# Optimization experiments

Hardware: AMD Instinct MI355X
Metric: run time of the kernel (lower is better)

## Reference

```python
import jax, jax.numpy as jnp
import numpy as np
from jax import lax


def _instance_loss(z1, z2, t):
    # z1, z2: [B,T,C]; t: [B,T] timestamps
    B, T, C = z1.shape
    if B == 1:
        return jnp.asarray(0.0, z1.dtype)
    N = B * T
    tf = t.reshape(N)
    diff = jnp.abs(tf[:, None] - tf[None, :])          # [N,N]
    seq = jnp.repeat(jnp.arange(B), T)                 # sequence id per row
    same_seq = seq[:, None] == seq[None, :]
    diff = jnp.where(same_seq, diff + diff.max() + 0.001, diff)
    # k=B smallest diffs per row (cross-sequence temporal neighbors)
    _, idx = lax.top_k(-diff, B)                       # [N,B]
    z1f = z1.reshape(N, C)
    z2f = z2.reshape(N, C)
    pos = jnp.sum(z1f * z2f, axis=-1)[:, None]         # [N,1]
    neg1 = jnp.einsum('nc,nkc->nk', z1f, z1f[idx])     # [N,B]
    neg2 = jnp.einsum('nc,nkc->nk', z1f, z2f[idx])     # [N,B]
    logits = jnp.concatenate([pos, neg1, neg2], axis=1)
    return -jax.nn.log_softmax(logits, axis=1)[:, 0].mean()


def _temporal_loss(z1, z2):
    B, T, C = z1.shape
    if T == 1:
        return jnp.asarray(0.0, z1.dtype)
    z = jnp.concatenate([z1, z2], axis=1)              # [B,2T,C]
    n = 2 * T
    sim = jnp.einsum('bic,bjc->bij', z, z)             # [B,2T,2T]
    # tril(sim,-1)[:,:,:-1] + triu(sim,1)[:,:,1:] == drop-diagonal shift
    i = jnp.arange(n)[:, None]
    j = jnp.arange(n - 1)[None, :]
    logits = jnp.where(j < i, sim[:, :, : n - 1], sim[:, :, 1:])  # [B,2T,2T-1]
    nls = -jax.nn.log_softmax(logits, axis=-1)
    tt = jnp.arange(T)
    return (nls[:, tt, T + tt - 1].mean() + nls[:, T + tt, tt].mean()) / 2


def _max_pool2(z):
    # F.max_pool1d(kernel=2, stride=2) over time axis (floor, drops odd tail)
    B, T, C = z.shape
    T2 = T // 2
    return z[:, : 2 * T2].reshape(B, T2, 2, C).max(axis=2)


def hierarchical_contrastive_loss(z1, z2, t, alpha=0.5, temporal_unit=0):
    B = z1.shape[0]
    loss = jnp.asarray(0.0, z1.dtype)
    d = 0
    while z1.shape[1] > 1:
        if alpha != 0:
            loss = loss + alpha * _instance_loss(z1, z2, t)
        if d >= temporal_unit and (1 - alpha) != 0:
            loss = loss + (1 - alpha) * _temporal_loss(z1, z2)
        d += 1
        z1 = _max_pool2(z1)
        z2 = _max_pool2(z2)
        Tt = t.shape[1]
        if Tt % 2 != 0:
            t = t[:, :-1]
        t = t.reshape(B, -1, 2).mean(axis=2)
    if z1.shape[1] == 1:
        if alpha != 0:
            loss = loss + alpha * _instance_loss(z1, z2, t)
        d += 1
    return loss / d


def setup_inputs() -> dict:
    key = jax.random.key(0)
    k1, k2, k3 = jax.random.split(key, 3)
    B, T, C = 8, 512, 320
    z1 = jax.random.normal(k1, (B, T, C), dtype=jnp.float32)
    z2 = jax.random.normal(k2, (B, T, C), dtype=jnp.float32)
    # irregular, increasing timestamps per sequence
    t = jnp.sort(jax.random.uniform(k3, (B, T), dtype=jnp.float32) * T, axis=1)
    return {"z1": z1, "z2": z2, "t": t}


def reference(z1, z2, t):
    return hierarchical_contrastive_loss(z1, z2, t, alpha=0.5, temporal_unit=0)
```

## Files before the change

kernel.cpp:

```cpp
#include <hip/hip_runtime.h>
#include <math.h>

#define BB 8
#define CC 320
#define ZB 2618880
#define TTOT 4088
#define NROWS 8184
#define NROWS_T 16352
#define NTBLK 440
#define PTOT 88032
#define XTOT 8176
#define NP1 327680
#define NP2 5120

#define FT 2618880
#define FPART 2622968
#define FROW 2799032
#define FCROSS 2823568

constexpr int kT[10]       = {512,256,128,64,32,16,8,4,2,1};
constexpr int kLogT[10]    = {9,8,7,6,5,4,3,2,1,0};
constexpr int kZBoff[10]   = {0,1310720,1966080,2293760,2457600,2539520,2580480,2600960,2611200,2616320};
constexpr int kToff[10]    = {0,0,2048,3072,3584,3840,3968,4032,4064,4080};
constexpr int kRowcum[11]  = {0,4096,6144,7168,7680,7936,8064,8128,8160,8176,8184};
constexpr int kTRowcum[10] = {0,8192,12288,14336,15360,15872,16128,16256,16320,16352};
constexpr int kNt128[9]    = {8,4,2,1,1,1,1,1,1};
constexpr int kLog128[9]   = {3,2,1,0,0,0,0,0,0};
constexpr int kPoff128[9]  = {0,65536,81920,86016,87040,87552,87808,87936,88000};
constexpr int kScount[9]   = {36,10,3,1,1,1,1,1,1};
constexpr int kSblkcum[10] = {0,288,368,392,400,408,416,424,432,440};
constexpr int kXoff[9]     = {0,4096,6144,7168,7680,7936,8064,8128,8160};

typedef short v8s __attribute__((ext_vector_type(8)));
typedef float v16f __attribute__((ext_vector_type(16)));

__device__ __forceinline__ unsigned short f2bf(float x) {
    unsigned int u = __float_as_uint(x);
    u = (u + 0x7FFFu + ((u >> 16) & 1u)) >> 16;
    return (unsigned short)u;
}
__device__ __forceinline__ float bfu(unsigned short u) {
    return __uint_as_float(((unsigned int)u) << 16);
}

__global__ void pool_lvl03(const float* __restrict__ z1,
                           const float* __restrict__ z2,
                           const float* __restrict__ t,
                           unsigned short* __restrict__ zb,
                           float* __restrict__ tpool) {
    int gid = blockIdx.x * 256 + threadIdx.x;
    if (gid < NP1) {
        int c = gid % CC;
        int rest = gid / CC;
        int ch = rest & 63;
        int b = (rest >> 6) & 7;
        int which = rest >> 9;
        const float* src =
            (which ? z2 : z1) + ((size_t)(b * 512 + ch * 8)) * CC + c;
        unsigned short* dst = zb + (size_t)which * ZB;
        float v[8];
#pragma unroll
        for (int j = 0; j < 8; j++) v[j] = src[(size_t)j * CC];
#pragma unroll
        for (int j = 0; j < 8; j++)
            dst[(size_t)(b * 512 + ch * 8 + j) * CC + c] = f2bf(v[j]);
        float m1[4];
#pragma unroll
        for (int j = 0; j < 4; j++) m1[j] = fmaxf(v[2 * j], v[2 * j + 1]);
#pragma unroll
        for (int j = 0; j < 4; j++)
            dst[kZBoff[1] + (size_t)(b * 256 + ch * 4 + j) * CC + c] =
                f2bf(m1[j]);
        float m2[2] = {fmaxf(m1[0], m1[1]), fmaxf(m1[2], m1[3])};
#pragma unroll
        for (int j = 0; j < 2; j++)
            dst[kZBoff[2] + (size_t)(b * 128 + ch * 2 + j) * CC + c] =
                f2bf(m2[j]);
        dst[kZBoff[3] + (size_t)(b * 64 + ch) * CC + c] =
            f2bf(fmaxf(m2[0], m2[1]));
    } else if (gid < NP1 + TTOT) {
        int i = gid - NP1;
        int l = 1;
#pragma unroll
        for (int q = 2; q <= 9; q++) l = (i >= kToff[q]) ? q : l;
        int rem = i - kToff[l];
        int Tl = kT[l];
        int t2 = rem & (Tl - 1);
        int b = rem >> kLogT[l];
        int win = 512 / Tl;
        const float* p = t + b * 512 + t2 * win;
        float s = 0.f;
        for (int j = 0; j < win; j++) s += p[j];
        tpool[kToff[l] + rem] = s * (1.0f / win);
    }
}

__global__ void pool_lvl49(unsigned short* __restrict__ zb) {
    int gid = blockIdx.x * 256 + threadIdx.x;
    if (gid >= NP2) return;
    int c = gid % CC;
    int r2 = gid / CC;
    int b = r2 & 7;
    int which = r2 >> 3;
    unsigned short* base = zb + (size_t)which * ZB;
    const unsigned short* src = base + kZBoff[3] + (size_t)(b * 64) * CC + c;
    float a[32];
#pragma unroll
    for (int j = 0; j < 32; j++)
        a[j] = fmaxf(bfu(src[(size_t)(2 * j) * CC]),
                     bfu(src[(size_t)(2 * j + 1) * CC]));
#pragma unroll
    for (int j = 0; j < 32; j++)
        base[kZBoff[4] + (size_t)(b * 32 + j) * CC + c] = f2bf(a[j]);
#pragma unroll
    for (int j = 0; j < 16; j++) a[j] = fmaxf(a[2 * j], a[2 * j + 1]);
#pragma unroll
    for (int j = 0; j < 16; j++)
        base[kZBoff[5] + (size_t)(b * 16 + j) * CC + c] = f2bf(a[j]);
#pragma unroll
    for (int j = 0; j < 8; j++) a[j] = fmaxf(a[2 * j], a[2 * j + 1]);
#pragma unroll
    for (int j = 0; j < 8; j++)
        base[kZBoff[6] + (size_t)(b * 8 + j) * CC + c] = f2bf(a[j]);
#pragma unroll
    for (int j = 0; j < 4; j++) a[j] = fmaxf(a[2 * j], a[2 * j + 1]);
#pragma unroll
    for (int j = 0; j < 4; j++)
        base[kZBoff[7] + (size_t)(b * 4 + j) * CC + c] = f2bf(a[j]);
#pragma unroll
    for (int j = 0; j < 2; j++) a[j] = fmaxf(a[2 * j], a[2 * j + 1]);
#pragma unroll
    for (int j = 0; j < 2; j++)
        base[kZBoff[8] + (size_t)(b * 2 + j) * CC + c] = f2bf(a[j]);
    base[kZBoff[9] + (size_t)b * CC + c] = f2bf(fmaxf(a[0], a[1]));
}

__global__ void topk_inst_all(const unsigned short* __restrict__ zb,
                              const float* __restrict__ t0,
                              const float* __restrict__ tpool,
                              float* __restrict__ rowloss) {
    int wave = threadIdx.x >> 6, lane = threadIdx.x & 63;
    int row = blockIdx.x * 4 + wave;
    if (row >= NROWS) return;
    int l = 0;
#pragma unroll
    for (int q = 1; q <= 9; q++) l = (row >= kRowcum[q]) ? q : l;
    int n = row - kRowcum[l];
    int T = kT[l];
    const float* tt = l ? tpool + kToff[l] : t0;
    int seq = n >> kLogT[l];
    float tn = tt[n];

    int idx8[8];
    if (lane < 8) {
        const float* ts = tt + lane * T;
        bool own = (lane == seq);
        int lo = 0, hi = T;
        while (lo < hi) {
            int mid = (lo + hi) >> 1;
            if (ts[mid] < tn) lo = mid + 1; else hi = mid;
        }
        int il = lo - 1, ih = lo;
        float dl = (il >= 0) ? (tn - ts[il]) : 3.0e38f;
        float dh = (ih < T) ? (ts[ih] - tn) : 3.0e38f;
#pragma unroll
        for (int r = 0; r < 8; r++) {
            bool pickLo = (dl <= dh);
            float dmin = own ? 1.0e12f : (pickLo ? dl : dh);
            int midx = own ? n : (lane * T + (pickLo ? il : ih));
            unsigned long long key =
                ((unsigned long long)__float_as_uint(dmin) << 32) |
                (unsigned int)midx;
            unsigned long long o;
            o = __shfl_xor(key, 1); key = (key < o) ? key : o;
            o = __shfl_xor(key, 2); key = (key < o) ? key : o;
            o = __shfl_xor(key, 4); key = (key < o) ? key : o;
            int widx = (int)(unsigned int)(key & 0xffffffffull);
            idx8[r] = widx;
            if (!own && widx == midx) {
                if (pickLo) { il--; dl = (il >= 0) ? (tn - ts[il]) : 3.0e38f; }
                else        { ih++; dh = (ih < T)  ? (ts[ih] - tn) : 3.0e38f; }
            }
        }
    }

    const unsigned short* z1 = zb + kZBoff[l];
    const unsigned short* z2 = zb + ZB + kZBoff[l];
    const unsigned short* z1n = z1 + (size_t)n * CC;
    const unsigned short* z2n = z2 + (size_t)n * CC;
    float a[5];
#pragma unroll
    for (int j = 0; j < 5; j++) a[j] = bfu(z1n[lane + 64 * j]);
    float part[17];
    {
        float s = 0.f;
#pragma unroll
        for (int j = 0; j < 5; j++) s += a[j] * bfu(z2n[lane + 64 * j]);
        part[0] = s;
    }
#pragma unroll
    for (int k = 0; k < 8; k++) {
        int p = __shfl(idx8[k], 0);
        const unsigned short* r1 = z1 + (size_t)p * CC;
        const unsigned short* r2 = z2 + (size_t)p * CC;
        float s1 = 0.f, s2 = 0.f;
#pragma unroll
        for (int j = 0; j < 5; j++) {
            float av = a[j];
            s1 += av * bfu(r1[lane + 64 * j]);
            s2 += av * bfu(r2[lane + 64 * j]);
        }
        part[1 + k] = s1;
        part[9 + k] = s2;
    }
#pragma unroll
    for (int q = 0; q < 17; q++) {
        float v = part[q];
        for (int off = 32; off > 0; off >>= 1) v += __shfl_xor(v, off);
        part[q] = v;
    }
    if (lane == 0) {
        float m = part[0];
#pragma unroll
        for (int q = 1; q < 17; q++) m = fmaxf(m, part[q]);
        float s = 0.f;
#pragma unroll
        for (int q = 0; q < 17; q++) s += expf(part[q] - m);
        float w = 0.05f / (float)(BB * T);
        rowloss[row] = w * (m + logf(s) - part[0]);
    }
}

__global__ void __launch_bounds__(256) temporal_mfma(
        const unsigned short* __restrict__ zb, float2* __restrict__ part,
        float* __restrict__ crossbuf) {
    int bid = blockIdx.x;
    int l = 0;
#pragma unroll
    for (int q = 1; q <= 8; q++) l = (bid >= kSblkcum[q]) ? q : l;
    int rem = bid - kSblkcum[l];
    int cnt = kScount[l];
    int Tl = kT[l], n = 2 * Tl, lnt = kLog128[l];
    int b = rem / cnt;
    int pr = rem - b * cnt;
    int rt = 0, width = kNt128[l];
    while (pr >= width) { pr -= width; rt++; width--; }
    int ct = rt + pr;
    bool diag = (rt == ct);
    const unsigned short* zb1 = zb + kZBoff[l] + (size_t)b * Tl * CC;
    const unsigned short* zb2 = zb + ZB + kZBoff[l] + (size_t)b * Tl * CC;
    int row0 = rt * 128, col0 = ct * 128;
    int tid = threadIdx.x;
    int w = tid >> 6, lane = tid & 63;
    __shared__ __align__(16) unsigned short As[4096];
    __shared__ __align__(16) unsigned short Bs[4096];
    __shared__ float2 cred[4][128];

    v16f acc[4];
#pragma unroll
    for (int cs = 0; cs < 4; cs++)
#pragma unroll
        for (int e = 0; e < 16; e++) acc[cs][e] = 0.f;

    int sofq[2]; const unsigned short* srcA[2]; const unsigned short* srcB[2];
    bool vA[2], vB[2];
#pragma unroll
    for (int q = 0; q < 2; q++) {
        int g = q * 256 + tid;
        int r = g & 127, kbb = g >> 7;
        sofq[q] = (r >> 5) * 1024 + (kbb >> 1) * 512 + (kbb & 1) * 256 +
                  (r & 31) * 8;
        int ka = kbb * 8;
        int gr = row0 + r;
        vA[q] = gr < n;
        srcA[q] = vA[q] ? ((gr < Tl) ? zb1 + (size_t)gr * CC + ka
                                     : zb2 + (size_t)(gr - Tl) * CC + ka)
                        : zb1;
        int gc = col0 + r;
        vB[q] = gc < n;
        srcB[q] = vB[q] ? ((gc < Tl) ? zb1 + (size_t)gc * CC + ka
                                     : zb2 + (size_t)(gc - Tl) * CC + ka)
                        : zb1;
    }

    for (int kc = 0; kc < CC; kc += 32) {
#pragma unroll
        for (int q = 0; q < 2; q++) {
            uint4 av = vA[q] ? *(const uint4*)(srcA[q] + kc)
                             : make_uint4(0, 0, 0, 0);
            *(uint4*)(As + sofq[q]) = av;
            if (!diag) {
                uint4 bv = vB[q] ? *(const uint4*)(srcB[q] + kc)
                                 : make_uint4(0, 0, 0, 0);
                *(uint4*)(Bs + sofq[q]) = bv;
            }
        }
        __syncthreads();
        const unsigned short* Ab = As + w * 1024;
        const unsigned short* Bb = diag ? As : Bs;
#pragma unroll
        for (int cc = 0; cc < 2; cc++) {
            v8s af = *(const v8s*)(Ab + cc * 512 + lane * 8);
#pragma unroll
            for (int cs = 0; cs < 4; cs++) {
                v8s bf = *(const v8s*)(Bb + cs * 1024 + cc * 512 + lane * 8);
                acc[cs] = __builtin_amdgcn_mfma_f32_32x32x16_bf16(
                    af, bf, acc[cs], 0, 0, 0);
            }
        }
        __syncthreads();
    }

    int colin = lane & 31;
    int rowhalf = 4 * (lane >> 5);

#pragma unroll
    for (int r = 0; r < 16; r++) {
        int lrow = (r & 3) + 8 * (r >> 2) + rowhalf;
        int grow = row0 + w * 32 + lrow;
        float vals[4];
        float lm = -3.0e38f;
#pragma unroll
        for (int cs = 0; cs < 4; cs++) {
            int gcol = col0 + cs * 32 + colin;
            float v = acc[cs][r];
            if (gcol >= n || gcol == grow) v = -3.0e38f;
            vals[cs] = v;
            lm = fmaxf(lm, v);
        }
#pragma unroll
        for (int off = 1; off < 32; off <<= 1)
            lm = fmaxf(lm, __shfl_xor(lm, off));
        float ls = 0.f;
#pragma unroll
        for (int cs = 0; cs < 4; cs++)
            ls += (vals[cs] > -1.0e38f) ? expf(vals[cs] - lm) : 0.f;
#pragma unroll
        for (int off = 1; off < 32; off <<= 1) ls += __shfl_xor(ls, off);
        if (colin == 0 && grow < n)
            part[kPoff128[l] + ((b * n + grow) << lnt) + ct] =
                make_float2(lm, ls);
    }

    if (ct - rt == (Tl >> 7)) {
#pragma unroll
        for (int r = 0; r < 16; r++) {
            int lrow = (r & 3) + 8 * (r >> 2) + rowhalf;
            int grow = row0 + w * 32 + lrow;
            if (grow < Tl) {
                int cidx = grow + Tl - col0;
                int cs_p = cidx >> 5, colin_p = cidx & 31;
                float cand = 0.f;
#pragma unroll
                for (int cs = 0; cs < 4; cs++)
                    cand += (cs == cs_p && colin == colin_p) ? acc[cs][r] : 0.f;
#pragma unroll
                for (int off = 1; off < 32; off <<= 1)
                    cand += __shfl_xor(cand, off);
                if (colin == 0)
                    crossbuf[kXoff[l] + b * Tl + grow] = cand;
            }
        }
    }

    if (!diag) {
#pragma unroll
        for (int cs = 0; cs < 4; cs++) {
            float m = acc[cs][0];
#pragma unroll
            for (int r = 1; r < 16; r++) m = fmaxf(m, acc[cs][r]);
            float mo = __shfl_xor(m, 32);
            float mm = fmaxf(m, mo);
            float s = 0.f;
#pragma unroll
            for (int r = 0; r < 16; r++) s += expf(acc[cs][r] - mm);
            s += __shfl_xor(s, 32);
            if (lane < 32) cred[w][cs * 32 + lane] = make_float2(mm, s);
        }
    }
    __syncthreads();
    if (!diag && tid < 128) {
        float2 a0 = cred[0][tid], a1 = cred[1][tid];
        float2 a2 = cred[2][tid], a3 = cred[3][tid];
        float M = fmaxf(fmaxf(a0.x, a1.x), fmaxf(a2.x, a3.x));
        float S = a0.y * expf(a0.x - M) + a1.y * expf(a1.x - M) +
                  a2.y * expf(a2.x - M) + a3.y * expf(a3.x - M);
        int gcol = col0 + tid;
        part[kPoff128[l] + ((b * n + gcol) << lnt) + rt] = make_float2(M, S);
    }
}

__global__ void merge_all(const float2* __restrict__ part,
                          const float* __restrict__ crossbuf,
                          float* __restrict__ rowloss) {
    int row = blockIdx.x * 256 + threadIdx.x;
    if (row >= NROWS_T) return;
    int l = 0;
#pragma unroll
    for (int q = 1; q <= 8; q++) l = (row >= kTRowcum[q]) ? q : l;
    int r = row - kTRowcum[l];
    int Tl = kT[l], n = 2 * Tl, nt = kNt128[l], lnt = kLog128[l];
    int b = r >> (kLogT[l] + 1);
    int rr = r & (n - 1);
    const float2* p = part + kPoff128[l] + ((size_t)(b * n + rr) << lnt);
    float M = -3.0e38f, S = 0.f;
    for (int k = 0; k < nt; k++) {
        float2 q = p[k];
        float nM = fmaxf(M, q.x);
        S = S * expf(M - nM) + q.y * expf(q.x - nM);
        M = nM;
    }
    float cross = crossbuf[kXoff[l] + b * Tl + (rr < Tl ? rr : rr - Tl)];
    float w = 0.025f / (float)(BB * Tl);
    rowloss[NROWS + row] = w * (M + logf(S) - cross);
}

__global__ void reduce_kernel(const float* __restrict__ rowloss,
                              float* __restrict__ out) {
    __shared__ float sm[16];
    int tid = threadIdx.x;
    float s = 0.f;
    for (int i = tid; i < NROWS + NROWS_T; i += 1024) s += rowloss[i];
#pragma unroll
    for (int off = 32; off > 0; off >>= 1) s += __shfl_xor(s, off);
    if ((tid & 63) == 0) sm[tid >> 6] = s;
    __syncthreads();
    if (tid < 64) {
        float v = (tid < 16) ? sm[tid] : 0.f;
#pragma unroll
        for (int off = 8; off > 0; off >>= 1) v += __shfl_xor(v, off);
        if (tid == 0) out[0] = v;
    }
}

extern "C" void kernel_launch(void* const* d_in, const int* in_sizes, int n_in,
                              void* d_out, int out_size, void* d_ws,
                              size_t ws_size, hipStream_t stream) {
    const float* z1 = (const float*)d_in[0];
    const float* z2 = (const float*)d_in[1];
    const float* t  = (const float*)d_in[2];
    float* ws = (float*)d_ws;
    unsigned short* zb = (unsigned short*)ws;
    float* tpool = ws + FT;
    float2* part = (float2*)(ws + FPART);
    float* rowloss = ws + FROW;
    float* crossbuf = ws + FCROSS;

    pool_lvl03<<<(NP1 + TTOT + 255) / 256, 256, 0, stream>>>(z1, z2, t, zb,
                                                             tpool);
    pool_lvl49<<<(NP2 + 255) / 256, 256, 0, stream>>>(zb);
    topk_inst_all<<<NROWS / 4, 256, 0, stream>>>(zb, t, tpool, rowloss);
    temporal_mfma<<<NTBLK, 256, 0, stream>>>(zb, part, crossbuf);
    merge_all<<<(NROWS_T + 255) / 256, 256, 0, stream>>>(part, crossbuf,
                                                         rowloss);
    reduce_kernel<<<1, 1024, 0, stream>>>(rowloss, (float*)d_out);
}
```

Before: 116.0 us.

## Fuse six launches into three: merged pooling, combined work kernel, last-block reduce

Folds the level 4-9 pooling into the first pooling kernel, recomputing it directly from the fp32 inputs with 16-row max windows. The temporal MFMA tiles and the instance top-k rows now run in one heterogeneous grid. Merge and final reduction use a last-block-done atomic counter. This cuts launch count and inter-kernel gaps and lets the two independent loss branches share the GPU, at the cost of more serial per-thread work in the new pooling path and an atomic counter that is reset inside the pooling kernel.

```diff
diff --git a/kernel.cpp b/kernel.cpp
--- a/kernel.cpp
+++ b/kernel.cpp
@@ -8,15 +8,16 @@
 #define NROWS 8184
 #define NROWS_T 16352
 #define NTBLK 440
-#define PTOT 88032
-#define XTOT 8176
 #define NP1 327680
 #define NP2 5120
+#define NMRB 64
 
 #define FT 2618880
 #define FPART 2622968
-#define FROW 2799032
-#define FCROSS 2823568
+#define FCROSS 2799032
+#define FROW 2807208
+#define FBLK 2815396
+#define FCNT 2815464
 
 constexpr int kT[10]       = {512,256,128,64,32,16,8,4,2,1};
 constexpr int kLogT[10]    = {9,8,7,6,5,4,3,2,1,0};
@@ -43,12 +44,14 @@
     return __uint_as_float(((unsigned int)u) << 16);
 }
 
-__global__ void pool_lvl03(const float* __restrict__ z1,
-                           const float* __restrict__ z2,
-                           const float* __restrict__ t,
-                           unsigned short* __restrict__ zb,
-                           float* __restrict__ tpool) {
+__global__ void pool_kernel(const float* __restrict__ z1,
+                            const float* __restrict__ z2,
+                            const float* __restrict__ t,
+                            unsigned short* __restrict__ zb,
+                            float* __restrict__ tpool,
+                            int* __restrict__ counter) {
     int gid = blockIdx.x * 256 + threadIdx.x;
+    if (gid == 0) *counter = 0;
     if (gid < NP1) {
         int c = gid % CC;
         int rest = gid / CC;
@@ -92,56 +95,54 @@
         float s = 0.f;
         for (int j = 0; j < win; j++) s += p[j];
         tpool[kToff[l] + rem] = s * (1.0f / win);
-    }
-}
-
-__global__ void pool_lvl49(unsigned short* __restrict__ zb) {
-    int gid = blockIdx.x * 256 + threadIdx.x;
-    if (gid >= NP2) return;
-    int c = gid % CC;
-    int r2 = gid / CC;
-    int b = r2 & 7;
-    int which = r2 >> 3;
-    unsigned short* base = zb + (size_t)which * ZB;
-    const unsigned short* src = base + kZBoff[3] + (size_t)(b * 64) * CC + c;
-    float a[32];
-#pragma unroll
-    for (int j = 0; j < 32; j++)
-        a[j] = fmaxf(bfu(src[(size_t)(2 * j) * CC]),
-                     bfu(src[(size_t)(2 * j + 1) * CC]));
-#pragma unroll
-    for (int j = 0; j < 32; j++)
-        base[kZBoff[4] + (size_t)(b * 32 + j) * CC + c] = f2bf(a[j]);
-#pragma unroll
-    for (int j = 0; j < 16; j++) a[j] = fmaxf(a[2 * j], a[2 * j + 1]);
-#pragma unroll
-    for (int j = 0; j < 16; j++)
-        base[kZBoff[5] + (size_t)(b * 16 + j) * CC + c] = f2bf(a[j]);
-#pragma unroll
-    for (int j = 0; j < 8; j++) a[j] = fmaxf(a[2 * j], a[2 * j + 1]);
-#pragma unroll
-    for (int j = 0; j < 8; j++)
-        base[kZBoff[6] + (size_t)(b * 8 + j) * CC + c] = f2bf(a[j]);
-#pragma unroll
-    for (int j = 0; j < 4; j++) a[j] = fmaxf(a[2 * j], a[2 * j + 1]);
-#pragma unroll
-    for (int j = 0; j < 4; j++)
-        base[kZBoff[7] + (size_t)(b * 4 + j) * CC + c] = f2bf(a[j]);
-#pragma unroll
-    for (int j = 0; j < 2; j++) a[j] = fmaxf(a[2 * j], a[2 * j + 1]);
-#pragma unroll
-    for (int j = 0; j < 2; j++)
-        base[kZBoff[8] + (size_t)(b * 2 + j) * CC + c] = f2bf(a[j]);
-    base[kZBoff[9] + (size_t)b * CC + c] = f2bf(fmaxf(a[0], a[1]));
-}
-
-__global__ void topk_inst_all(const unsigned short* __restrict__ zb,
-                              const float* __restrict__ t0,
-                              const float* __restrict__ tpool,
-                              float* __restrict__ rowloss) {
-    int wave = threadIdx.x >> 6, lane = threadIdx.x & 63;
-    int row = blockIdx.x * 4 + wave;
-    if (row >= NROWS) return;
+    } else if (gid < NP1 + TTOT + NP2) {
+        int i = gid - (NP1 + TTOT);
+        int c = i % CC;
+        int r2 = i / CC;
+        int b = r2 & 7;
+        int which = r2 >> 3;
+        const float* src = (which ? z2 : z1) + (size_t)(b * 512) * CC + c;
+        unsigned short* base = zb + (size_t)which * ZB;
+        float a5 = 0.f, a6 = 0.f, a7 = 0.f, a8 = 0.f, a9 = 0.f;
+        for (int g = 0; g < 32; g++) {
+            float m = src[(size_t)(g * 16) * CC];
+            for (int r = 1; r < 16; r++)
+                m = fmaxf(m, src[(size_t)(g * 16 + r) * CC]);
+            base[kZBoff[4] + (size_t)(b * 32 + g) * CC + c] = f2bf(m);
+            a5 = (g & 1) ? fmaxf(a5, m) : m;
+            if (g & 1) {
+                int j5 = g >> 1;
+                base[kZBoff[5] + (size_t)(b * 16 + j5) * CC + c] = f2bf(a5);
+                a6 = (j5 & 1) ? fmaxf(a6, a5) : a5;
+                if (j5 & 1) {
+                    int j6 = j5 >> 1;
+                    base[kZBoff[6] + (size_t)(b * 8 + j6) * CC + c] = f2bf(a6);
+                    a7 = (j6 & 1) ? fmaxf(a7, a6) : a6;
+                    if (j6 & 1) {
+                        int j7 = j6 >> 1;
+                        base[kZBoff[7] + (size_t)(b * 4 + j7) * CC + c] =
+                            f2bf(a7);
+                        a8 = (j7 & 1) ? fmaxf(a8, a7) : a7;
+                        if (j7 & 1) {
+                            int j8 = j7 >> 1;
+                            base[kZBoff[8] + (size_t)(b * 2 + j8) * CC + c] =
+                                f2bf(a8);
+                            a9 = (j8 & 1) ? fmaxf(a9, a8) : a8;
+                            if (j8 & 1)
+                                base[kZBoff[9] + (size_t)b * CC + c] =
+                                    f2bf(a9);
+                        }
+                    }
+                }
+            }
+        }
+    }
+}
+
+__device__ __forceinline__ void d_topk_row(
+        int row, const unsigned short* __restrict__ zb,
+        const float* __restrict__ t0, const float* __restrict__ tpool,
+        int lane, float* local) {
     int l = 0;
 #pragma unroll
     for (int q = 1; q <= 9; q++) l = (row >= kRowcum[q]) ? q : l;
@@ -227,14 +228,14 @@
 #pragma unroll
         for (int q = 0; q < 17; q++) s += expf(part[q] - m);
         float w = 0.05f / (float)(BB * T);
-        rowloss[row] = w * (m + logf(s) - part[0]);
-    }
-}
-
-__global__ void __launch_bounds__(256) temporal_mfma(
-        const unsigned short* __restrict__ zb, float2* __restrict__ part,
-        float* __restrict__ crossbuf) {
-    int bid = blockIdx.x;
+        *local += w * (m + logf(s) - part[0]);
+    }
+}
+
+__device__ __forceinline__ void d_temporal_tile(
+        int bid, const unsigned short* __restrict__ zb,
+        float2* __restrict__ part, float* __restrict__ crossbuf,
+        char* smem, int tid) {
     int l = 0;
 #pragma unroll
     for (int q = 1; q <= 8; q++) l = (bid >= kSblkcum[q]) ? q : l;
@@ -250,11 +251,10 @@
     const unsigned short* zb1 = zb + kZBoff[l] + (size_t)b * Tl * CC;
     const unsigned short* zb2 = zb + ZB + kZBoff[l] + (size_t)b * Tl * CC;
     int row0 = rt * 128, col0 = ct * 128;
-    int tid = threadIdx.x;
     int w = tid >> 6, lane = tid & 63;
-    __shared__ __align__(16) unsigned short As[4096];
-    __shared__ __align__(16) unsigned short Bs[4096];
-    __shared__ float2 cred[4][128];
+    unsigned short* As = (unsigned short*)smem;
+    unsigned short* Bs = (unsigned short*)(smem + 8192);
+    float2* cred = (float2*)smem;
 
     v16f acc[4];
 #pragma unroll
@@ -375,13 +375,13 @@
 #pragma unroll
             for (int r = 0; r < 16; r++) s += expf(acc[cs][r] - mm);
             s += __shfl_xor(s, 32);
-            if (lane < 32) cred[w][cs * 32 + lane] = make_float2(mm, s);
+            if (lane < 32) cred[w * 128 + cs * 32 + lane] = make_float2(mm, s);
         }
     }
     __syncthreads();
     if (!diag && tid < 128) {
-        float2 a0 = cred[0][tid], a1 = cred[1][tid];
-        float2 a2 = cred[2][tid], a3 = cred[3][tid];
+        float2 a0 = cred[0 * 128 + tid], a1 = cred[1 * 128 + tid];
+        float2 a2 = cred[2 * 128 + tid], a3 = cred[3 * 128 + tid];
         float M = fmaxf(fmaxf(a0.x, a1.x), fmaxf(a2.x, a3.x));
         float S = a0.y * expf(a0.x - M) + a1.y * expf(a1.x - M) +
                   a2.y * expf(a2.x - M) + a3.y * expf(a3.x - M);
@@ -390,11 +390,26 @@
     }
 }
 
-__global__ void merge_all(const float2* __restrict__ part,
-                          const float* __restrict__ crossbuf,
-                          float* __restrict__ rowloss) {
-    int row = blockIdx.x * 256 + threadIdx.x;
-    if (row >= NROWS_T) return;
+__global__ void __launch_bounds__(256) work_kernel(
+        const unsigned short* __restrict__ zb, const float* __restrict__ t0,
+        const float* __restrict__ tpool, float2* __restrict__ part,
+        float* __restrict__ crossbuf, float* __restrict__ rowloss) {
+    __shared__ __align__(16) char smem[16512];
+    int bid = blockIdx.x, tid = threadIdx.x;
+    if (bid < NTBLK) {
+        d_temporal_tile(bid, zb, part, crossbuf, smem, tid);
+    } else {
+        int wave = tid >> 6, lane = tid & 63;
+        int row = (bid - NTBLK) * 4 + wave;
+        float loc = 0.f;
+        d_topk_row(row, zb, t0, tpool, lane, &loc);
+        if (lane == 0) rowloss[row] = loc;
+    }
+}
+
+__device__ __forceinline__ void d_merge_row(
+        int row, const float2* __restrict__ part,
+        const float* __restrict__ crossbuf, float* local) {
     int l = 0;
 #pragma unroll
     for (int q = 1; q <= 8; q++) l = (row >= kTRowcum[q]) ? q : l;
@@ -405,30 +420,46 @@
     const float2* p = part + kPoff128[l] + ((size_t)(b * n + rr) << lnt);
     float M = -3.0e38f, S = 0.f;
     for (int k = 0; k < nt; k++) {
-        float2 q = p[k];
-        float nM = fmaxf(M, q.x);
-        S = S * expf(M - nM) + q.y * expf(q.x - nM);
+        float2 q2 = p[k];
+        float nM = fmaxf(M, q2.x);
+        S = S * expf(M - nM) + q2.y * expf(q2.x - nM);
         M = nM;
     }
     float cross = crossbuf[kXoff[l] + b * Tl + (rr < Tl ? rr : rr - Tl)];
     float w = 0.025f / (float)(BB * Tl);
-    rowloss[NROWS + row] = w * (M + logf(S) - cross);
-}
-
-__global__ void reduce_kernel(const float* __restrict__ rowloss,
-                              float* __restrict__ out) {
-    __shared__ float sm[16];
-    int tid = threadIdx.x;
-    float s = 0.f;
-    for (int i = tid; i < NROWS + NROWS_T; i += 1024) s += rowloss[i];
-#pragma unroll
-    for (int off = 32; off > 0; off >>= 1) s += __shfl_xor(s, off);
-    if ((tid & 63) == 0) sm[tid >> 6] = s;
+    *local += w * (M + logf(S) - cross);
+}
+
+__global__ void merge_reduce_kernel(const float2* __restrict__ part,
+                                    const float* __restrict__ crossbuf,
+                                    const float* __restrict__ rowloss,
+                                    float* __restrict__ blockpart,
+                                    int* __restrict__ counter,
+                                    float* __restrict__ out) {
+    __shared__ float redsm[4];
+    __shared__ int flag;
+    int bid = blockIdx.x, tid = threadIdx.x;
+    int gid = bid * 256 + tid;
+    int wave = tid >> 6, lane = tid & 63;
+    float local = 0.f;
+    if (gid < NROWS_T) d_merge_row(gid, part, crossbuf, &local);
+    if (gid < NROWS) local += rowloss[gid];
+#pragma unroll
+    for (int off = 32; off > 0; off >>= 1) local += __shfl_xor(local, off);
+    if (lane == 0) redsm[wave] = local;
     __syncthreads();
-    if (tid < 64) {
-        float v = (tid < 16) ? sm[tid] : 0.f;
-#pragma unroll
-        for (int off = 8; off > 0; off >>= 1) v += __shfl_xor(v, off);
+    if (tid == 0) {
+        float bs = redsm[0] + redsm[1] + redsm[2] + redsm[3];
+        atomicExch(blockpart + bid, bs);
+        __threadfence();
+        int old = atomicAdd(counter, 1);
+        flag = (old == NMRB - 1) ? 1 : 0;
+    }
+    __syncthreads();
+    if (flag && tid < 64) {
+        float v = atomicAdd(blockpart + tid, 0.0f);
+#pragma unroll
+        for (int off = 32; off > 0; off >>= 1) v += __shfl_xor(v, off);
         if (tid == 0) out[0] = v;
     }
 }
@@ -443,15 +474,17 @@
     unsigned short* zb = (unsigned short*)ws;
     float* tpool = ws + FT;
     float2* part = (float2*)(ws + FPART);
+    float* crossbuf = ws + FCROSS;
     float* rowloss = ws + FROW;
-    float* crossbuf = ws + FCROSS;
-
-    pool_lvl03<<<(NP1 + TTOT + 255) / 256, 256, 0, stream>>>(z1, z2, t, zb,
-                                                             tpool);
-    pool_lvl49<<<(NP2 + 255) / 256, 256, 0, stream>>>(zb);
-    topk_inst_all<<<NROWS / 4, 256, 0, stream>>>(zb, t, tpool, rowloss);
-    temporal_mfma<<<NTBLK, 256, 0, stream>>>(zb, part, crossbuf);
-    merge_all<<<(NROWS_T + 255) / 256, 256, 0, stream>>>(part, crossbuf,
-                                                         rowloss);
-    reduce_kernel<<<1, 1024, 0, stream>>>(rowloss, (float*)d_out);
-}
+    float* blockpart = ws + FBLK;
+    int* counter = (int*)(ws + FCNT);
+    float* out = (float*)d_out;
+
+    int np = NP1 + TTOT + NP2;
+    pool_kernel<<<(np + 255) / 256, 256, 0, stream>>>(z1, z2, t, zb, tpool,
+                                                      counter);
+    work_kernel<<<NTBLK + NROWS / 4, 256, 0, stream>>>(zb, t, tpool, part,
+                                                       crossbuf, rowloss);
+    merge_reduce_kernel<<<NMRB, 256, 0, stream>>>(part, crossbuf, rowloss,
+                                                  blockpart, counter, out);
+}
```

Measured after the change: 123.5 us. 6.4% more time.

## Fuse merge and final reduction into one last-block-done kernel

Applied to the files above, without the earlier changes.

Merges the per-row temporal logsumexp merge and the global sum into one kernel that uses per-block partials and an atomic counter, so the last block finishes the reduction. This removes a separate single-block reduce launch. The temporal kernel also aliases its shared reduction buffer onto the A/B tile memory to cut LDS use, and its block-index decode changes from a divide to a shift/mask. The counter is reset in the first pool kernel, and correctness relies on fence and atomic ordering across blocks.

```diff
diff --git a/kernel.cpp b/kernel.cpp
--- a/kernel.cpp
+++ b/kernel.cpp
@@ -8,15 +8,16 @@
 #define NROWS 8184
 #define NROWS_T 16352
 #define NTBLK 440
-#define PTOT 88032
-#define XTOT 8176
 #define NP1 327680
 #define NP2 5120
+#define NMRB 64
 
 #define FT 2618880
 #define FPART 2622968
-#define FROW 2799032
-#define FCROSS 2823568
+#define FCROSS 2799032
+#define FROW 2807208
+#define FBLK 2815396
+#define FCNT 2815464
 
 constexpr int kT[10]       = {512,256,128,64,32,16,8,4,2,1};
 constexpr int kLogT[10]    = {9,8,7,6,5,4,3,2,1,0};
@@ -27,7 +28,6 @@
 constexpr int kNt128[9]    = {8,4,2,1,1,1,1,1,1};
 constexpr int kLog128[9]   = {3,2,1,0,0,0,0,0,0};
 constexpr int kPoff128[9]  = {0,65536,81920,86016,87040,87552,87808,87936,88000};
-constexpr int kScount[9]   = {36,10,3,1,1,1,1,1,1};
 constexpr int kSblkcum[10] = {0,288,368,392,400,408,416,424,432,440};
 constexpr int kXoff[9]     = {0,4096,6144,7168,7680,7936,8064,8128,8160};
 
@@ -43,12 +43,14 @@
     return __uint_as_float(((unsigned int)u) << 16);
 }
 
-__global__ void pool_lvl03(const float* __restrict__ z1,
-                           const float* __restrict__ z2,
-                           const float* __restrict__ t,
-                           unsigned short* __restrict__ zb,
-                           float* __restrict__ tpool) {
+__global__ void pool03_kernel(const float* __restrict__ z1,
+                              const float* __restrict__ z2,
+                              const float* __restrict__ t,
+                              unsigned short* __restrict__ zb,
+                              float* __restrict__ tpool,
+                              int* __restrict__ counter) {
     int gid = blockIdx.x * 256 + threadIdx.x;
+    if (gid == 0) *counter = 0;
     if (gid < NP1) {
         int c = gid % CC;
         int rest = gid / CC;
@@ -95,7 +97,7 @@
     }
 }
 
-__global__ void pool_lvl49(unsigned short* __restrict__ zb) {
+__global__ void pool49_kernel(unsigned short* __restrict__ zb) {
     int gid = blockIdx.x * 256 + threadIdx.x;
     if (gid >= NP2) return;
     int c = gid % CC;
@@ -135,10 +137,10 @@
     base[kZBoff[9] + (size_t)b * CC + c] = f2bf(fmaxf(a[0], a[1]));
 }
 
-__global__ void topk_inst_all(const unsigned short* __restrict__ zb,
-                              const float* __restrict__ t0,
-                              const float* __restrict__ tpool,
-                              float* __restrict__ rowloss) {
+__global__ void topk_kernel(const unsigned short* __restrict__ zb,
+                            const float* __restrict__ t0,
+                            const float* __restrict__ tpool,
+                            float* __restrict__ rowloss) {
     int wave = threadIdx.x >> 6, lane = threadIdx.x & 63;
     int row = blockIdx.x * 4 + wave;
     if (row >= NROWS) return;
@@ -231,18 +233,18 @@
     }
 }
 
-__global__ void __launch_bounds__(256) temporal_mfma(
+__global__ void __launch_bounds__(256) temporal_kernel(
         const unsigned short* __restrict__ zb, float2* __restrict__ part,
         float* __restrict__ crossbuf) {
-    int bid = blockIdx.x;
+    __shared__ __align__(16) char smem[16512];
+    int bid = blockIdx.x, tid = threadIdx.x;
     int l = 0;
 #pragma unroll
     for (int q = 1; q <= 8; q++) l = (bid >= kSblkcum[q]) ? q : l;
     int rem = bid - kSblkcum[l];
-    int cnt = kScount[l];
+    int b = rem & 7;
+    int pr = rem >> 3;
     int Tl = kT[l], n = 2 * Tl, lnt = kLog128[l];
-    int b = rem / cnt;
-    int pr = rem - b * cnt;
     int rt = 0, width = kNt128[l];
     while (pr >= width) { pr -= width; rt++; width--; }
     int ct = rt + pr;
@@ -250,11 +252,10 @@
     const unsigned short* zb1 = zb + kZBoff[l] + (size_t)b * Tl * CC;
     const unsigned short* zb2 = zb + ZB + kZBoff[l] + (size_t)b * Tl * CC;
     int row0 = rt * 128, col0 = ct * 128;
-    int tid = threadIdx.x;
     int w = tid >> 6, lane = tid & 63;
-    __shared__ __align__(16) unsigned short As[4096];
-    __shared__ __align__(16) unsigned short Bs[4096];
-    __shared__ float2 cred[4][128];
+    unsigned short* As = (unsigned short*)smem;
+    unsigned short* Bs = (unsigned short*)(smem + 8192);
+    float2* cred = (float2*)smem;
 
     v16f acc[4];
 #pragma unroll
@@ -375,13 +376,13 @@
 #pragma unroll
             for (int r = 0; r < 16; r++) s += expf(acc[cs][r] - mm);
             s += __shfl_xor(s, 32);
-            if (lane < 32) cred[w][cs * 32 + lane] = make_float2(mm, s);
+            if (lane < 32) cred[w * 128 + cs * 32 + lane] = make_float2(mm, s);
         }
     }
     __syncthreads();
     if (!diag && tid < 128) {
-        float2 a0 = cred[0][tid], a1 = cred[1][tid];
-        float2 a2 = cred[2][tid], a3 = cred[3][tid];
+        float2 a0 = cred[0 * 128 + tid], a1 = cred[1 * 128 + tid];
+        float2 a2 = cred[2 * 128 + tid], a3 = cred[3 * 128 + tid];
         float M = fmaxf(fmaxf(a0.x, a1.x), fmaxf(a2.x, a3.x));
         float S = a0.y * expf(a0.x - M) + a1.y * expf(a1.x - M) +
                   a2.y * expf(a2.x - M) + a3.y * expf(a3.x - M);
@@ -390,11 +391,9 @@
     }
 }
 
-__global__ void merge_all(const float2* __restrict__ part,
-                          const float* __restrict__ crossbuf,
-                          float* __restrict__ rowloss) {
-    int row = blockIdx.x * 256 + threadIdx.x;
-    if (row >= NROWS_T) return;
+__device__ __forceinline__ void d_merge_row(
+        int row, const float2* __restrict__ part,
+        const float* __restrict__ crossbuf, float* local) {
     int l = 0;
 #pragma unroll
     for (int q = 1; q <= 8; q++) l = (row >= kTRowcum[q]) ? q : l;
@@ -405,30 +404,46 @@
     const float2* p = part + kPoff128[l] + ((size_t)(b * n + rr) << lnt);
     float M = -3.0e38f, S = 0.f;
     for (int k = 0; k < nt; k++) {
-        float2 q = p[k];
-        float nM = fmaxf(M, q.x);
-        S = S * expf(M - nM) + q.y * expf(q.x - nM);
+        float2 q2 = p[k];
+        float nM = fmaxf(M, q2.x);
+        S = S * expf(M - nM) + q2.y * expf(q2.x - nM);
         M = nM;
     }
     float cross = crossbuf[kXoff[l] + b * Tl + (rr < Tl ? rr : rr - Tl)];
     float w = 0.025f / (float)(BB * Tl);
-    rowloss[NROWS + row] = w * (M + logf(S) - cross);
-}
-
-__global__ void reduce_kernel(const float* __restrict__ rowloss,
-                              float* __restrict__ out) {
-    __shared__ float sm[16];
-    int tid = threadIdx.x;
-    float s = 0.f;
-    for (int i = tid; i < NROWS + NROWS_T; i += 1024) s += rowloss[i];
-#pragma unroll
-    for (int off = 32; off > 0; off >>= 1) s += __shfl_xor(s, off);
-    if ((tid & 63) == 0) sm[tid >> 6] = s;
+    *local += w * (M + logf(S) - cross);
+}
+
+__global__ void merge_reduce_kernel(const float2* __restrict__ part,
+                                    const float* __restrict__ crossbuf,
+                                    const float* __restrict__ rowloss,
+                                    float* __restrict__ blockpart,
+                                    int* __restrict__ counter,
+                                    float* __restrict__ out) {
+    __shared__ float redsm[4];
+    __shared__ int flag;
+    int bid = blockIdx.x, tid = threadIdx.x;
+    int gid = bid * 256 + tid;
+    int wave = tid >> 6, lane = tid & 63;
+    float local = 0.f;
+    if (gid < NROWS_T) d_merge_row(gid, part, crossbuf, &local);
+    if (gid < NROWS) local += rowloss[gid];
+#pragma unroll
+    for (int off = 32; off > 0; off >>= 1) local += __shfl_xor(local, off);
+    if (lane == 0) redsm[wave] = local;
     __syncthreads();
-    if (tid < 64) {
-        float v = (tid < 16) ? sm[tid] : 0.f;
-#pragma unroll
-        for (int off = 8; off > 0; off >>= 1) v += __shfl_xor(v, off);
+    if (tid == 0) {
+        float bs = redsm[0] + redsm[1] + redsm[2] + redsm[3];
+        atomicExch(blockpart + bid, bs);
+        __threadfence();
+        int old = atomicAdd(counter, 1);
+        flag = (old == NMRB - 1) ? 1 : 0;
+    }
+    __syncthreads();
+    if (flag && tid < 64) {
+        float v = atomicAdd(blockpart + tid, 0.0f);
+#pragma unroll
+        for (int off = 32; off > 0; off >>= 1) v += __shfl_xor(v, off);
         if (tid == 0) out[0] = v;
     }
 }
@@ -443,15 +458,17 @@
     unsigned short* zb = (unsigned short*)ws;
     float* tpool = ws + FT;
     float2* part = (float2*)(ws + FPART);
+    float* crossbuf = ws + FCROSS;
     float* rowloss = ws + FROW;
-    float* crossbuf = ws + FCROSS;
-
-    pool_lvl03<<<(NP1 + TTOT + 255) / 256, 256, 0, stream>>>(z1, z2, t, zb,
-                                                             tpool);
-    pool_lvl49<<<(NP2 + 255) / 256, 256, 0, stream>>>(zb);
-    topk_inst_all<<<NROWS / 4, 256, 0, stream>>>(zb, t, tpool, rowloss);
-    temporal_mfma<<<NTBLK, 256, 0, stream>>>(zb, part, crossbuf);
-    merge_all<<<(NROWS_T + 255) / 256, 256, 0, stream>>>(part, crossbuf,
-                                                         rowloss);
-    reduce_kernel<<<1, 1024, 0, stream>>>(rowloss, (float*)d_out);
-}
+    float* blockpart = ws + FBLK;
+    int* counter = (int*)(ws + FCNT);
+    float* out = (float*)d_out;
+
+    pool03_kernel<<<(NP1 + TTOT + 255) / 256, 256, 0, stream>>>(
+        z1, z2, t, zb, tpool, counter);
+    pool49_kernel<<<(NP2 + 255) / 256, 256, 0, stream>>>(zb);
+    topk_kernel<<<NROWS / 4, 256, 0, stream>>>(zb, t, tpool, rowloss);
+    temporal_kernel<<<NTBLK, 256, 0, stream>>>(zb, part, crossbuf);
+    merge_reduce_kernel<<<NMRB, 256, 0, stream>>>(part, crossbuf, rowloss,
+                                                  blockpart, counter, out);
+}
```

New measurement: 106.9 us. 1.09x faster.
